# Kernel optimization log

Hardware: AMD Instinct MI355X
Metric: run time of the kernel (lower is better)

Reference implementation:

```python
import jax, jax.numpy as jnp
import numpy as np

B, H, W, IN, HID, L, M1, M2, OUT, NT = 32, 128, 256, 4, 64, 4, 12, 12, 2, 14


def setup_inputs() -> dict:
    key = jax.random.key(0)
    ks = jax.random.split(key, 32)
    f32 = jnp.float32
    n = lambda k, s, scale=0.02: jax.random.normal(k, s, dtype=f32) * scale
    inp = jax.random.normal(ks[0], (B, H, W, IN), dtype=f32)
    # ext: [B,1,6]; col0 float feature, col2 day idx in [0,8), col3 hour idx in [5,19)
    c0 = jax.random.uniform(ks[1], (B, 1), dtype=f32)
    c1 = jax.random.uniform(ks[2], (B, 1), dtype=f32)
    c2 = jax.random.randint(ks[3], (B, 1), 0, 8).astype(f32)
    c3 = jax.random.randint(ks[4], (B, 1), 5, 19).astype(f32)
    c45 = jax.random.uniform(ks[5], (B, 2), dtype=f32)
    ext = jnp.concatenate([c0, c1, c2, c3, c45], axis=1)[:, None, :]
    return {
        'inp': inp, 'ext': ext,
        'enc_w': n(ks[6], (HID, IN + 1)), 'enc_b': n(ks[7], (HID,)),
        'w1r': n(ks[8], (L, HID, HID, M1, M2), 1.0 / (HID * HID)),
        'w1i': n(ks[9], (L, HID, HID, M1, M2), 1.0 / (HID * HID)),
        'w2r': n(ks[10], (L, HID, HID, M1, M2), 1.0 / (HID * HID)),
        'w2i': n(ks[11], (L, HID, HID, M1, M2), 1.0 / (HID * HID)),
        'ws_w': n(ks[12], (L, HID, HID)), 'ws_b': n(ks[13], (L, HID)),
        'day_emb': n(ks[14], (8, 2), 1.0), 'hour_emb': n(ks[15], (24, 3), 1.0),
        'e1_w': n(ks[16], (64, 6)), 'e1_b': n(ks[17], (64,)),
        'e2_w': n(ks[18], (H * W, 64)), 'e2_b': n(ks[19], (H * W,)),
        'tw': n(ks[20], (NT, HID, HID, 3, 3)), 'tb': n(ks[21], (NT, HID)),
        'f1_w': n(ks[22], (128, HID)), 'f1_b': n(ks[23], (128,)),
        'f2_w': n(ks[24], (HID, 128)), 'f2_b': n(ks[25], (HID,)),
        'f3_w': n(ks[26], (OUT, HID)), 'f3_b': n(ks[27], (OUT,)),
    }


def _act(x):
    return jax.nn.gelu(x, approximate=False)  # torch nn.GELU default (erf)


def _spectral(x, w1, w2):
    # x: [b,c,h,w]; w1,w2: complex [c_in,c_out,M1,M2]
    b, c, h, w = x.shape
    xft = jnp.fft.rfft2(x)  # [b,c,h,w//2+1]
    out = jnp.zeros((b, w1.shape[1], h, w // 2 + 1), dtype=xft.dtype)
    out = out.at[:, :, :M1, :M2].set(
        jnp.einsum('bixy,ioxy->boxy', xft[:, :, :M1, :M2], w1))
    out = out.at[:, :, -M1:, :M2].set(
        jnp.einsum('bixy,ioxy->boxy', xft[:, :, -M1:, :M2], w2))
    return jnp.fft.irfft2(out, s=(h, w))


def reference(inp, ext, enc_w, enc_b, w1r, w1i, w2r, w2i, ws_w, ws_b,
              day_emb, hour_emb, e1_w, e1_b, e2_w, e2_b, tw, tb,
              f1_w, f1_b, f2_w, f2_b, f3_w, f3_b):
    b, h, w, _ = inp.shape
    e = ext[:, 0, :]  # squeeze(1) -> [b,6]
    # embed_ext: [ext0, day_emb, hour_emb] -> [b,6]
    emb = jnp.concatenate([
        e[:, 0:1],
        day_emb[e[:, 2].astype(jnp.int32)],
        hour_emb[e[:, 3].astype(jnp.int32)],
    ], axis=1)
    # ext2lr_global (dropout = identity in eval)
    g = _act(emb @ e1_w.T + e1_b)
    g = _act(g @ e2_w.T + e2_b).reshape(b, h, w, 1)
    x = jnp.concatenate([inp, g], axis=-1)          # [b,h,w,IN+1]
    x = (x @ enc_w.T + enc_b).transpose(0, 3, 1, 2)  # [b,HID,h,w]
    # FNO integral layers
    for i in range(L):
        x1 = _spectral(x, w1r[i] + 1j * w1i[i], w2r[i] + 1j * w2i[i])
        x2 = jnp.einsum('bchw,oc->bohw', x, ws_w[i]) + ws_b[i][None, :, None, None]
        x = x1 + x2
        if i != L - 1:
            x = _act(x)
    # decoder_time: per-sample expert conv selected by hour index
    t = e[:, 3].astype(jnp.int32) - 5  # in [0, NT)
    Wt, bt = tw[t], tb[t]              # [b,HID,HID,3,3], [b,HID]
    def one(xi, wi, bi):
        y = jax.lax.conv_general_dilated(
            xi[None], wi, (1, 1), 'SAME',
            dimension_numbers=('NCHW', 'OIHW', 'NCHW'))[0]
        return y + bi[:, None, None]
    hfeat = _act(jax.vmap(one)(x, Wt, bt)).transpose(0, 2, 3, 1)  # [b,h,w,HID]
    # decoder MLP
    z = _act(hfeat @ f1_w.T + f1_b)
    z = _act(z @ f2_w.T + f2_b)
    return z @ f3_w.T + f3_b  # [b,h,w,OUT]
```

## Files before the change

kernel.cpp:

```cpp
#include <hip/hip_runtime.h>
#include <math.h>

#define BB 32
#define HH_ 128
#define WW_ 256

typedef _Float16 f16_t;
typedef _Float16 half8 __attribute__((ext_vector_type(8)));
typedef _Float16 half4 __attribute__((ext_vector_type(4)));
typedef float floatx4 __attribute__((ext_vector_type(4)));

__device__ __forceinline__ float gelu_f(float v){
  float t = v * 0.70710678118654752f;
  float s = __builtin_fabsf(t);
  float k = __builtin_amdgcn_rcpf(__builtin_fmaf(0.3275911f, s, 1.0f));
  float p = __builtin_fmaf(1.061405429f, k, -1.453152027f);
  p = __builtin_fmaf(p, k, 1.421413741f);
  p = __builtin_fmaf(p, k, -0.284496736f);
  p = __builtin_fmaf(p, k, 0.254829592f);
  p = p * k;
  float e = __expf(-t * t);
  float erfa = __builtin_fmaf(-p, e, 1.0f);
  float er = __builtin_copysignf(erfa, v);
  float vh = 0.5f * v;
  return __builtin_fmaf(vh, er, vh);
}

__global__ void k_diag(float* out, float v){ out[threadIdx.x] = v; }

__global__ __launch_bounds__(256) void k_prep(
      float2* twf, float2* thf, float2* thi, f16_t* twzh,
      const float* __restrict__ f1_w, const float* __restrict__ f2_w,
      const float* __restrict__ f3_w, f16_t* f1T, f16_t* f2T, f16_t* f3T,
      const float* __restrict__ tw, f16_t* __restrict__ wT,
      const float* __restrict__ w1r, const float* __restrict__ w1i,
      const float* __restrict__ w2r, const float* __restrict__ w2i,
      float2* __restrict__ wmix, f16_t* __restrict__ twA){
  __shared__ __align__(16) char smp[53248];
  const double PI2 = 6.283185307179586476925286766559;
  int blk = blockIdx.x, tid = threadIdx.x;
  if (blk < 113){
    int t = blk*256 + tid;
    if (t < 3072){
      int w = t/12, ky = t%12;
      double a = -PI2 * (double)(w*ky) / 256.0;
      twf[t] = make_float2((float)cos(a), (float)sin(a));
    } else if (t < 6144){
      int f = t-3072; int h = f/24, j = f%24;
      int kx = (j<12)? j : j+104;
      double a = -PI2 * (double)(h*kx) / 128.0;
      thf[f] = make_float2((float)cos(a), (float)sin(a));
    } else if (t < 9216){
      int f = t-6144; int h = f/24, j = f%24;
      int kx = (j<12)? j : j+104;
      double a = PI2 * (double)(h*kx) / 128.0;
      thi[f] = make_float2((float)(cos(a)/128.0), (float)(sin(a)/128.0));
    } else if (t < 12288){
      int f = t-9216; int w = f/12, ky = f%12;
      double a = PI2 * (double)(w*ky) / 256.0;
      double s = (ky==0)? 1.0 : 2.0;
      twzh[w*32 + ky]      = (f16_t)( s*cos(a)/256.0);
      twzh[w*32 + 12 + ky] = (f16_t)(-s*sin(a)/256.0);
      if (ky < 8) twzh[w*32 + 24 + ky] = (f16_t)0.f;
    } else {
      int t2 = t - 12288;
      if (t2 < 8192) f1T[t2] = (f16_t)f1_w[t2];
      else if (t2 < 16384) f2T[t2-8192] = (f16_t)f2_w[t2-8192];
      else if (t2 < 16512) f3T[t2-16384] = (f16_t)f3_w[t2-16384];
    }
  } else if (blk < 169){
    float* s = (float*)smp;
    int b2 = blk - 113;
    int og = b2 & 3, tt = b2 >> 2;
    const float* src = tw + (long)tt*36864 + og*9216;
    for (int f = tid; f < 9216; f += 256) s[f] = src[f];
    __syncthreads();
    for (int f = tid; f < 9216; f += 256){
      int c = f & 63; int r = f >> 6;
      int o16 = r % 16, tap = r / 16;
      float v = s[(o16*64 + c)*9 + tap];
      wT[(((long)tt*9 + tap)*64 + og*16 + o16)*64 + c] = (f16_t)v;
    }
  } else if (blk < 937){
    float* sr = (float*)smp;
    float* si = (float*)(smp + 26624);
    int b2 = blk - 169;
    int ig  = b2 & 7;
    int kx  = (b2 >> 3) % 12;
    int sel = (b2 / 96) & 1;
    int l   = b2 / 192;
    const float* wr = sel ? w2r : w1r;
    const float* wi = sel ? w2i : w1i;
    for (int f = tid; f < 6144; f += 256){
      int i8 = f / 768; int rem = f % 768;
      int o = rem / 12, ky = rem % 12;
      long addr = (((long)l*64 + ig*8 + i8)*64 + o)*144 + kx*12 + ky;
      sr[(i8*64 + o)*13 + ky] = wr[addr];
      si[(i8*64 + o)*13 + ky] = wi[addr];
    }
    __syncthreads();
    int j = sel ? (kx + 12) : kx;
    for (int f = tid; f < 6144; f += 256){
      int o = f & 63; int r = f >> 6;
      int ky = r % 12, i8 = r / 12;
      int sidx = (i8*64 + o)*13 + ky;
      wmix[(((long)l*288 + j*12 + ky))*4096 + (ig*8 + i8)*64 + o] =
          make_float2(sr[sidx], si[sidx]);
    }
  } else {
    int t = (blk - 937)*256 + tid;
    int halfi = t >> 13, r = t & 8191;
    int hl = r >> 12, r2 = r & 4095;
    int m = r2 >> 7, k = r2 & 127;
    f16_t v = (f16_t)0.f;
    if (m < 24){
      int ky = m >> 1, ri = m & 1;
      int w = halfi*128 + k;
      double a = -PI2 * (double)(w*ky) / 256.0;
      float t32 = (float)(ri ? sin(a) : cos(a));
      f16_t hi = (f16_t)t32;
      v = hl ? (f16_t)(t32 - (float)hi) : hi;
    }
    twA[t] = v;
  }
}

__global__ __launch_bounds__(256) void k_gxdft(const float* __restrict__ ext,
      const float* __restrict__ day_emb, const float* __restrict__ hour_emb,
      const float* __restrict__ e1_w, const float* __restrict__ e1_b,
      const float* __restrict__ e2_w, const float* __restrict__ e2_b,
      const float* __restrict__ inp, const float* __restrict__ enc_w,
      const float* __restrict__ enc_b, const f16_t* __restrict__ twA,
      f16_t* __restrict__ x, float2* __restrict__ fp0, float2* __restrict__ fp1){
  __shared__ __align__(16) char sm[59392];
  f16_t* Obt   = (f16_t*)sm;
  f16_t* twA_l = (f16_t*)(sm + 35072);
  float* gvs   = (float*)(sm + 52480);
  float4* ips  = (float4*)(sm + 53504);
  float* s     = (float*)(sm + 57600);
  float* ew    = (float*)(sm + 57856);
  float* eb    = (float*)(sm + 59136);
  int tid = threadIdx.x;
  int bh = blockIdx.x;
  int b = bh >> 7, h = bh & 127;
  if (tid < 64){
    int j = tid;
    const float* e = ext + b*6;
    float emb[6];
    emb[0] = e[0];
    int d  = (int)e[2];
    emb[1] = day_emb[d*2];  emb[2] = day_emb[d*2+1];
    int hr = (int)e[3];
    emb[3] = hour_emb[hr*3]; emb[4] = hour_emb[hr*3+1]; emb[5] = hour_emb[hr*3+2];
    float acc = e1_b[j];
    #pragma unroll
    for (int k = 0; k < 6; k++) acc += emb[k]*e1_w[j*6+k];
    s[j] = gelu_f(acc);
    eb[j] = enc_b[j];
  }
  for (int f = tid; f < 320; f += 256) ew[f] = enc_w[f];
  __syncthreads();
  {
    int px = tid;
    long hw = (long)h*256 + px;
    const float4* wrow = (const float4*)(e2_w + hw*64);
    float acc = e2_b[hw];
    #pragma unroll
    for (int k = 0; k < 16; k++){
      float4 v = wrow[k];
      acc += v.x*s[4*k] + v.y*s[4*k+1] + v.z*s[4*k+2] + v.w*s[4*k+3];
    }
    gvs[px] = gelu_f(acc);
    ips[px] = *(const float4*)(inp + ((long)b*32768 + hw)*4);
  }
  __syncthreads();
  int lane = tid & 63, wv = tid >> 6;
  {
    int c = lane, wg = wv;
    const float* wr2 = ew + c*5;
    float w0 = wr2[0], w1 = wr2[1], w2 = wr2[2], w3 = wr2[3], w4 = wr2[4];
    float ebc = eb[c];
    f16_t* xo = x + ((long)bh*256 + wg*64)*64 + c;
    #pragma unroll 2
    for (int g8 = 0; g8 < 8; g8++){
      half8 hv;
      #pragma unroll
      for (int e2 = 0; e2 < 8; e2++){
        int i = g8*8 + e2;
        float4 ip = ips[wg*64 + i];
        float gv = gvs[wg*64 + i];
        float v = ebc + ip.x*w0 + ip.y*w1 + ip.z*w2 + ip.w*w3 + gv*w4;
        f16_t hval = (f16_t)v;
        hv[e2] = hval;
        xo[i*64] = hval;
      }
      *(half8*)(Obt + c*274 + wg*64 + g8*8) = hv;
    }
  }
  for (int f = tid; f < 1024; f += 256){
    int hl = f >> 9, m = (f >> 4) & 31, kc8 = f & 15;
    *(float4*)(twA_l + hl*4352 + m*136 + kc8*8) = *(const float4*)(twA + f*8);
  }
  __syncthreads();
  int n15 = lane & 15, quad = lane >> 4;
  int n = wv*16 + n15;
  #pragma unroll
  for (int half = 0; half < 2; half++){
    if (half == 1){
      __syncthreads();
      for (int f = tid; f < 1024; f += 256){
        int hl = f >> 9, m = (f >> 4) & 31, kc8 = f & 15;
        *(float4*)(twA_l + hl*4352 + m*136 + kc8*8) =
            *(const float4*)(twA + 8192 + f*8);
      }
      __syncthreads();
    }
    half8 bfr2[4];
    #pragma unroll
    for (int ks = 0; ks < 4; ks++)
      bfr2[ks] = *(const half8*)(Obt + n*274 + half*128 + ks*32 + quad*8);
    floatx4 dacc[2];
    dacc[0] = (floatx4){0.f,0.f,0.f,0.f};
    dacc[1] = (floatx4){0.f,0.f,0.f,0.f};
    #pragma unroll
    for (int hl = 0; hl < 2; hl++){
      #pragma unroll
      for (int mt = 0; mt < 2; mt++){
        #pragma unroll
        for (int ks = 0; ks < 4; ks++){
          half8 a = *(const half8*)(twA_l + hl*4352 + (mt*16 + n15)*136
                                    + ks*32 + quad*8);
          dacc[mt] = __builtin_amdgcn_mfma_f32_16x16x32_f16(a, bfr2[ks],
                                                            dacc[mt], 0,0,0);
        }
      }
    }
    float2* dst = half ? fp1 : fp0;
    #pragma unroll
    for (int mt = 0; mt < 2; mt++){
      int m0 = mt*16 + quad*4;
      if (m0 < 24){
        int ky0 = m0 >> 1;
        dst[(long)bh*768 + ky0*64 + n]     = make_float2(dacc[mt][0], dacc[mt][1]);
        dst[(long)bh*768 + (ky0+1)*64 + n] = make_float2(dacc[mt][2], dacc[mt][3]);
      }
    }
  }
}

__global__ __launch_bounds__(256) void k_spec(const float2* __restrict__ s0,
      const float2* __restrict__ s1, int dual, const float2* __restrict__ thf_g,
      const float2* __restrict__ thi_g, const float2* __restrict__ wmix,
      int layer, float2* __restrict__ zi){
  __shared__ __align__(16) char sm[40960];
  float2* th  = (float2*)sm;
  float2* xch = (float2*)(sm + 24576);
  float2* mixL= (float2*)(sm + 24576);
  int tid = threadIdx.x;
  int b = blockIdx.x / 12, ky = blockIdx.x % 12;
  int wv = tid >> 6, lane = tid & 63;
  for (int f = tid; f < 3072; f += 256) th[f] = thf_g[f];
  float2 acc[6];
  #pragma unroll
  for (int q = 0; q < 6; q++) acc[q] = make_float2(0.f, 0.f);
  long base = (long)b*98304 + ky*64;
  for (int ch = 0; ch < 4; ch++){
    __syncthreads();
    for (int f = tid; f < 2048; f += 256){
      int hh = f >> 6, c = f & 63;
      long idx = base + (long)(ch*32 + hh)*768 + c;
      float2 v = s0[idx];
      if (dual){ float2 u = s1[idx]; v.x += u.x; v.y += u.y; }
      xch[f] = v;
    }
    __syncthreads();
    for (int hh = 0; hh < 32; hh++){
      float2 v = xch[hh*64 + lane];
      int hg = ch*32 + hh;
      #pragma unroll
      for (int q = 0; q < 6; q++){
        float2 t = th[hg*24 + q*4 + wv];
        acc[q].x += t.x*v.x - t.y*v.y;
        acc[q].y += t.x*v.y + t.y*v.x;
      }
    }
  }
  __syncthreads();
  for (int f = tid; f < 3072; f += 256) th[f] = thi_g[f];
  float2 mout[6];
  #pragma unroll
  for (int q = 0; q < 6; q++){
    int j = q*4 + wv;
    const float2* wj = wmix + (((long)layer*288 + j*12 + ky))*4096;
    float re = 0.f, im = 0.f;
    #pragma unroll 8
    for (int i = 0; i < 64; i++){
      float vr = __shfl(acc[q].x, i);
      float vi = __shfl(acc[q].y, i);
      float2 ww = wj[i*64 + lane];
      re += vr*ww.x - vi*ww.y;
      im += vr*ww.y + vi*ww.x;
    }
    mout[q] = make_float2(re, im);
  }
  #pragma unroll
  for (int q = 0; q < 6; q++) mixL[(q*4 + wv)*64 + lane] = mout[q];
  __syncthreads();
  float2 cr[24];
  #pragma unroll
  for (int j = 0; j < 24; j++) cr[j] = mixL[j*64 + lane];
  for (int qq = 0; qq < 32; qq++){
    int h = qq*4 + wv;
    float re = 0.f, im = 0.f;
    #pragma unroll
    for (int j = 0; j < 24; j++){
      float2 t = th[h*24 + j];
      re += t.x*cr[j].x - t.y*cr[j].y;
      im += t.x*cr[j].y + t.y*cr[j].x;
    }
    zi[((long)b*128 + h)*768 + ky*64 + lane] = make_float2(re, im);
  }
}

__global__ __launch_bounds__(256) void k_iw_mfma(f16_t* __restrict__ x,
      const float2* __restrict__ zi, const float* __restrict__ ws_w,
      const float* __restrict__ ws_b, const f16_t* __restrict__ twzh,
      const f16_t* __restrict__ twA, float2* __restrict__ fp0,
      float2* __restrict__ fp1, int layer, int act, int dodft){
  __shared__ __align__(16) char sm[52736];
  f16_t* A  = (f16_t*)sm;
  f16_t* Bm = (f16_t*)(sm + 34816);
  float* sb = (float*)(sm + 52224);
  f16_t* Obt  = (f16_t*)sm;
  f16_t* twA_l= (f16_t*)(sm + 17408);
  int tid = threadIdx.x;
  int blk = blockIdx.x;
  int half = blk & 1;
  long bh = blk >> 1;
  int w0 = half*128;
  const f16_t* xrow = x + (bh*256 + w0)*64;
  for (int f = tid; f < 1024; f += 256){
    int px = f >> 3, c8 = (f & 7)*8;
    *(float4*)((char*)A + (px*136 + c8)*2) = *(const float4*)(xrow + px*64 + c8);
  }
  for (int f = tid; f < 4096; f += 256){
    int px = f >> 5, k = f & 31;
    if (k < 24){
      f16_t v = twzh[(w0+px)*32 + k];
      A[px*136 + 64 + k] = v;
      A[px*136 + 88 + k] = v;
      A[px*136 + 112 + k] = (f16_t)0.f;
    }
  }
  const float* wsl = ws_w + (long)layer*4096;
  for (int f = tid; f < 1024; f += 256){
    int o = f >> 4, c4 = f & 15;
    float4 v = *(const float4*)(wsl + o*64 + c4*4);
    f16_t* d = Bm + o*136 + c4*4;
    d[0]=(f16_t)v.x; d[1]=(f16_t)v.y; d[2]=(f16_t)v.z; d[3]=(f16_t)v.w;
  }
  const float2* zrow = zi + bh*768;
  for (int f = tid; f < 768; f += 256){
    int o = f & 63, ky = f >> 6;
    float2 v = zrow[ky*64 + o];
    f16_t hr = (f16_t)v.x; f16_t hi_ = (f16_t)v.y;
    Bm[o*136 + 64 + ky] = hr;
    Bm[o*136 + 76 + ky] = hi_;
    Bm[o*136 + 88 + ky] = (f16_t)(v.x - (float)hr);
    Bm[o*136 +100 + ky] = (f16_t)(v.y - (float)hi_);
  }
  for (int f = tid; f < 2048; f += 256){
    int o = f >> 5, k = f & 31;
    if (k < 24) Bm[o*136 + 112 + k] = (f16_t)0.f;
  }
  if (tid < 64) sb[tid] = ws_b[layer*64 + tid];
  __syncthreads();
  int lane = tid & 63, wv = tid >> 6;
  int n15 = lane & 15, quad = lane >> 4;
  int n = wv*16 + n15;
  half8 bfr[4];
  #pragma unroll
  for (int kc = 0; kc < 4; kc++)
    bfr[kc] = *(const half8*)(Bm + n*136 + kc*32 + quad*8);
  floatx4 acc[8];
  #pragma unroll
  for (int mt = 0; mt < 8; mt++){
    floatx4 c = {0.f,0.f,0.f,0.f};
    #pragma unroll
    for (int kc = 0; kc < 4; kc++){
      half8 a = *(const half8*)(A + (mt*16 + n15)*136 + kc*32 + quad*8);
      c = __builtin_amdgcn_mfma_f32_16x16x32_f16(a, bfr[kc], c, 0, 0, 0);
    }
    acc[mt] = c;
  }
  float bias = sb[n];
  __syncthreads();
  f16_t* xo = x + (bh*256 + w0)*64;
  #pragma unroll
  for (int mt = 0; mt < 8; mt++){
    half4 hv;
    #pragma unroll
    for (int r = 0; r < 4; r++){
      float v = acc[mt][r] + bias;
      if (act) v = gelu_f(v);
      hv[r] = (f16_t)v;
      xo[(mt*16 + quad*4 + r)*64 + n] = hv[r];
    }
    if (dodft) *(half4*)(Obt + n*136 + mt*16 + quad*4) = hv;
  }
  if (dodft){
    const f16_t* tsrc = twA + half*8192;
    for (int f = tid; f < 1024; f += 256){
      int hl = f >> 9, m = (f >> 4) & 31, kc8 = f & 15;
      *(float4*)(twA_l + hl*4352 + m*136 + kc8*8) = *(const float4*)(tsrc + f*8);
    }
    __syncthreads();
    half8 bfr2[4];
    #pragma unroll
    for (int ks = 0; ks < 4; ks++)
      bfr2[ks] = *(const half8*)(Obt + n*136 + ks*32 + quad*8);
    floatx4 dacc[2];
    dacc[0] = (floatx4){0.f,0.f,0.f,0.f};
    dacc[1] = (floatx4){0.f,0.f,0.f,0.f};
    #pragma unroll
    for (int hl = 0; hl < 2; hl++){
      #pragma unroll
      for (int mt = 0; mt < 2; mt++){
        #pragma unroll
        for (int ks = 0; ks < 4; ks++){
          half8 a = *(const half8*)(twA_l + hl*4352 + (mt*16 + n15)*136
                                    + ks*32 + quad*8);
          dacc[mt] = __builtin_amdgcn_mfma_f32_16x16x32_f16(a, bfr2[ks],
                                                            dacc[mt], 0,0,0);
        }
      }
    }
    float2* dst = half ? fp1 : fp0;
    #pragma unroll
    for (int mt = 0; mt < 2; mt++){
      int m0 = mt*16 + quad*4;
      if (m0 < 24){
        int ky0 = m0 >> 1;
        dst[bh*768 + ky0*64 + n]     = make_float2(dacc[mt][0], dacc[mt][1]);
        dst[bh*768 + (ky0+1)*64 + n] = make_float2(dacc[mt][2], dacc[mt][3]);
      }
    }
  }
}

__global__ __launch_bounds__(256) void k_conv_head(const f16_t* __restrict__ x,
      const float* __restrict__ ext, const f16_t* __restrict__ wT,
      const float* __restrict__ tb, const f16_t* __restrict__ f1T,
      const float* __restrict__ f1_b, const f16_t* __restrict__ f2T,
      const float* __restrict__ f2_b, const f16_t* __restrict__ f3T,
      const float* __restrict__ f3_b, float* __restrict__ out){
  __shared__ __align__(16) char sm[29824];
  f16_t* hf   = (f16_t*)sm;
  f16_t* z1   = (f16_t*)(sm + 9216);
  f16_t* z2   = (f16_t*)sm;
  float* tbs  = (float*)(sm + 28512);
  float* f1bs = (float*)(sm + 28768);
  float* f2bs = (float*)(sm + 29280);
  f16_t* f3s  = (f16_t*)(sm + 29536);
  float* f3bs = (float*)(sm + 29792);
  f16_t* xt   = (f16_t*)sm;

  int tid = threadIdx.x;
  int blk = blockIdx.x;
  int wc = blk & 3, h = (blk >> 2) & 127, b = blk >> 9;
  int w0 = wc*64;
  int t_idx = (int)ext[b*6+3] - 5;

  if (tid < 64) tbs[tid] = tb[t_idx*64 + tid];
  else if (tid < 192) f1bs[tid-64] = f1_b[tid-64];
  else f2bs[tid-192] = f2_b[tid-192];
  if (tid < 128) f3s[tid] = f3T[tid];
  if (tid < 2) f3bs[tid] = f3_b[tid];

  for (int f = tid; f < 1584; f += 256){
    int c8 = f & 7, r = f >> 3;
    int dy = r/66, pxl = r%66;
    int hh = h - 1 + dy, wg = w0 - 1 + pxl;
    float4 v = {0.f,0.f,0.f,0.f};
    if (hh >= 0 && hh < HH_ && wg >= 0 && wg < WW_)
      v = *(const float4*)(x + (((long)b*HH_ + hh)*WW_ + wg)*64 + c8*8);
    *(float4*)(xt + (dy*66 + pxl)*72 + c8*8) = v;
  }
  __syncthreads();

  int lane = tid & 63, wv = tid >> 6;
  int n15 = lane & 15, quad = lane >> 4;

  floatx4 acc[4];
  #pragma unroll
  for (int mt = 0; mt < 4; mt++) acc[mt] = (floatx4){0.f,0.f,0.f,0.f};
  const f16_t* wTt = wT + (long)t_idx*36864;
  for (int tap = 0; tap < 9; tap++){
    int dy = tap/3, dx = tap%3;
    const f16_t* wrow = wTt + (tap*64 + wv*16 + n15)*64;
    #pragma unroll
    for (int kc = 0; kc < 2; kc++){
      half8 bfrag = *(const half8*)(wrow + kc*32 + quad*8);
      #pragma unroll
      for (int mt = 0; mt < 4; mt++){
        int p = mt*16 + n15 + dx;
        half8 a = *(const half8*)(xt + (dy*66 + p)*72 + kc*32 + quad*8);
        acc[mt] = __builtin_amdgcn_mfma_f32_16x16x32_f16(a, bfrag, acc[mt], 0,0,0);
      }
    }
  }
  __syncthreads();
  {
    int n = wv*16 + n15;
    float bias = tbs[n];
    #pragma unroll
    for (int mt = 0; mt < 4; mt++){
      #pragma unroll
      for (int r = 0; r < 4; r++){
        int m = mt*16 + quad*4 + r;
        hf[m*72 + n] = (f16_t)gelu_f(acc[mt][r] + bias);
      }
    }
  }
  __syncthreads();
  #pragma unroll
  for (int nt = 0; nt < 2; nt++){
    int n = wv*32 + nt*16 + n15;
    float bias = f1bs[n];
    half8 bf0 = *(const half8*)(f1T + n*64 + quad*8);
    half8 bf1 = *(const half8*)(f1T + n*64 + 32 + quad*8);
    #pragma unroll
    for (int mt = 0; mt < 4; mt++){
      floatx4 c = {0.f,0.f,0.f,0.f};
      half8 a0 = *(const half8*)(hf + (mt*16 + n15)*72 + quad*8);
      half8 a1 = *(const half8*)(hf + (mt*16 + n15)*72 + 32 + quad*8);
      c = __builtin_amdgcn_mfma_f32_16x16x32_f16(a0, bf0, c, 0,0,0);
      c = __builtin_amdgcn_mfma_f32_16x16x32_f16(a1, bf1, c, 0,0,0);
      #pragma unroll
      for (int r = 0; r < 4; r++){
        int m = mt*16 + quad*4 + r;
        z1[m*136 + n] = (f16_t)gelu_f(c[r] + bias);
      }
    }
  }
  __syncthreads();
  {
    int n = wv*16 + n15;
    float bias = f2bs[n];
    half8 bf[4];
    #pragma unroll
    for (int kc = 0; kc < 4; kc++)
      bf[kc] = *(const half8*)(f2T + n*128 + kc*32 + quad*8);
    #pragma unroll
    for (int mt = 0; mt < 4; mt++){
      floatx4 c = {0.f,0.f,0.f,0.f};
      #pragma unroll
      for (int kc = 0; kc < 4; kc++){
        half8 a = *(const half8*)(z1 + (mt*16 + n15)*136 + kc*32 + quad*8);
        c = __builtin_amdgcn_mfma_f32_16x16x32_f16(a, bf[kc], c, 0,0,0);
      }
      #pragma unroll
      for (int r = 0; r < 4; r++){
        int m = mt*16 + quad*4 + r;
        z2[m*72 + n] = (f16_t)gelu_f(c[r] + bias);
      }
    }
  }
  __syncthreads();
  if (tid < 128){
    int px = tid >> 1, oo = tid & 1;
    const f16_t* zr = z2 + px*72;
    const f16_t* fr = f3s + oo*64;
    float a = f3bs[oo];
    #pragma unroll
    for (int g = 0; g < 8; g++){
      half8 zv = *(const half8*)(zr + g*8);
      half8 wv2 = *(const half8*)(fr + g*8);
      #pragma unroll
      for (int q = 0; q < 8; q++) a += (float)zv[q]*(float)wv2[q];
    }
    out[(((long)b*HH_ + h)*WW_ + w0 + px)*2 + oo] = a;
  }
}

extern "C" void kernel_launch(void* const* d_in, const int* in_sizes, int n_in,
                              void* d_out, int out_size, void* d_ws, size_t ws_size,
                              hipStream_t stream){
  const float* inp     = (const float*)d_in[0];
  const float* ext     = (const float*)d_in[1];
  const float* enc_w   = (const float*)d_in[2];
  const float* enc_b   = (const float*)d_in[3];
  const float* w1r     = (const float*)d_in[4];
  const float* w1i     = (const float*)d_in[5];
  const float* w2r     = (const float*)d_in[6];
  const float* w2i     = (const float*)d_in[7];
  const float* ws_w    = (const float*)d_in[8];
  const float* ws_b    = (const float*)d_in[9];
  const float* day_emb = (const float*)d_in[10];
  const float* hour_emb= (const float*)d_in[11];
  const float* e1_w    = (const float*)d_in[12];
  const float* e1_b    = (const float*)d_in[13];
  const float* e2_w    = (const float*)d_in[14];
  const float* e2_b    = (const float*)d_in[15];
  const float* tw      = (const float*)d_in[16];
  const float* tb      = (const float*)d_in[17];
  const float* f1_w    = (const float*)d_in[18];
  const float* f1_b    = (const float*)d_in[19];
  const float* f2_w    = (const float*)d_in[20];
  const float* f2_b    = (const float*)d_in[21];
  const float* f3_w    = (const float*)d_in[22];
  const float* f3_b    = (const float*)d_in[23];
  float* outp = (float*)d_out;

  const size_t need = 248652032;
  if (ws_size < need){
    k_diag<<<dim3(1), dim3(64), 0, stream>>>(outp, (float)(ws_size >> 20));
    return;
  }
  char* p = (char*)d_ws;
  f16_t*  x    = (f16_t*)(p);
  float2* fp0  = (float2*)(p + 134217728);
  float2* fp1  = (float2*)(p + 159383552);
  float2* zi   = (float2*)(p + 184549376);
  float2* twf  = (float2*)(p + 209715200);
  float2* thf  = (float2*)(p + 209739776);
  float2* thi  = (float2*)(p + 209764352);
  f16_t*  twzh = (f16_t*)(p + 209788928);
  f16_t*  wT   = (f16_t*)(p + 209805312);
  f16_t*  f1T  = (f16_t*)(p + 210837504);
  f16_t*  f2T  = (f16_t*)(p + 210853888);
  f16_t*  f3T  = (f16_t*)(p + 210870272);
  float2* wmix = (float2*)(p + 210870528);
  f16_t*  twA  = (f16_t*)(p + 248619264);

  k_prep<<<dim3(1001), dim3(256), 0, stream>>>(twf, thf, thi, twzh,
      f1_w, f2_w, f3_w, f1T, f2T, f3T, tw, wT, w1r, w1i, w2r, w2i, wmix, twA);
  k_gxdft<<<dim3(4096), dim3(256), 0, stream>>>(ext, day_emb, hour_emb,
      e1_w, e1_b, e2_w, e2_b, inp, enc_w, enc_b, twA, x, fp0, fp1);
  for (int l = 0; l < 4; l++){
    k_spec<<<dim3(384), dim3(256), 0, stream>>>(fp0, fp1, 1,
                                                thf, thi, wmix, l, zi);
    k_iw_mfma<<<dim3(8192), dim3(256), 0, stream>>>(x, zi, ws_w, ws_b, twzh,
                       twA, fp0, fp1, l, (l < 3) ? 1 : 0, (l < 3) ? 1 : 0);
  }
  k_conv_head<<<dim3(16384), dim3(256), 0, stream>>>(x, ext, wT, tb,
                     f1T, f1_b, f2T, f2_b, f3T, f3_b, outp);
}
```

Measured before the change: 1.289 ms.

## Read DFT twiddles from global, restructure integral-layer MFMA, trim LDS and GELU

After: 1.200 ms. 6.9% less time.

```diff
diff --git a/kernel.cpp b/kernel.cpp
--- a/kernel.cpp
+++ b/kernel.cpp
@@ -8,22 +8,21 @@
 typedef _Float16 f16_t;
 typedef _Float16 half8 __attribute__((ext_vector_type(8)));
 typedef _Float16 half4 __attribute__((ext_vector_type(4)));
+typedef _Float16 half2v __attribute__((ext_vector_type(2)));
 typedef float floatx4 __attribute__((ext_vector_type(4)));
 
 __device__ __forceinline__ float gelu_f(float v){
-  float t = v * 0.70710678118654752f;
-  float s = __builtin_fabsf(t);
+  float av = __builtin_fabsf(v);
+  float s = av * 0.70710678118654752f;
   float k = __builtin_amdgcn_rcpf(__builtin_fmaf(0.3275911f, s, 1.0f));
   float p = __builtin_fmaf(1.061405429f, k, -1.453152027f);
   p = __builtin_fmaf(p, k, 1.421413741f);
   p = __builtin_fmaf(p, k, -0.284496736f);
   p = __builtin_fmaf(p, k, 0.254829592f);
   p = p * k;
-  float e = __expf(-t * t);
-  float erfa = __builtin_fmaf(-p, e, 1.0f);
-  float er = __builtin_copysignf(erfa, v);
-  float vh = 0.5f * v;
-  return __builtin_fmaf(vh, er, vh);
+  float e = __expf(-s * s);
+  float q = 0.5f * av * p;
+  return __builtin_fmaf(-q, e, fmaxf(v, 0.f));
 }
 
 __global__ void k_diag(float* out, float v){ out[threadIdx.x] = v; }
@@ -132,14 +131,13 @@
       const float* __restrict__ inp, const float* __restrict__ enc_w,
       const float* __restrict__ enc_b, const f16_t* __restrict__ twA,
       f16_t* __restrict__ x, float2* __restrict__ fp0, float2* __restrict__ fp1){
-  __shared__ __align__(16) char sm[59392];
+  __shared__ __align__(16) char sm[41984];
   f16_t* Obt   = (f16_t*)sm;
-  f16_t* twA_l = (f16_t*)(sm + 35072);
-  float* gvs   = (float*)(sm + 52480);
-  float4* ips  = (float4*)(sm + 53504);
-  float* s     = (float*)(sm + 57600);
-  float* ew    = (float*)(sm + 57856);
-  float* eb    = (float*)(sm + 59136);
+  float* gvs   = (float*)(sm + 35072);
+  float4* ips  = (float4*)(sm + 36096);
+  float* s     = (float*)(sm + 40192);
+  float* ew    = (float*)(sm + 40448);
+  float* eb    = (float*)(sm + 41728);
   int tid = threadIdx.x;
   int bh = blockIdx.x;
   int b = bh >> 7, h = bh & 127;
@@ -197,24 +195,11 @@
       *(half8*)(Obt + c*274 + wg*64 + g8*8) = hv;
     }
   }
-  for (int f = tid; f < 1024; f += 256){
-    int hl = f >> 9, m = (f >> 4) & 31, kc8 = f & 15;
-    *(float4*)(twA_l + hl*4352 + m*136 + kc8*8) = *(const float4*)(twA + f*8);
-  }
   __syncthreads();
   int n15 = lane & 15, quad = lane >> 4;
   int n = wv*16 + n15;
   #pragma unroll
   for (int half = 0; half < 2; half++){
-    if (half == 1){
-      __syncthreads();
-      for (int f = tid; f < 1024; f += 256){
-        int hl = f >> 9, m = (f >> 4) & 31, kc8 = f & 15;
-        *(float4*)(twA_l + hl*4352 + m*136 + kc8*8) =
-            *(const float4*)(twA + 8192 + f*8);
-      }
-      __syncthreads();
-    }
     half8 bfr2[4];
     #pragma unroll
     for (int ks = 0; ks < 4; ks++)
@@ -228,8 +213,8 @@
       for (int mt = 0; mt < 2; mt++){
         #pragma unroll
         for (int ks = 0; ks < 4; ks++){
-          half8 a = *(const half8*)(twA_l + hl*4352 + (mt*16 + n15)*136
-                                    + ks*32 + quad*8);
+          half8 a = *(const half8*)(twA + half*8192 + hl*4096
+                                    + (mt*16 + n15)*128 + ks*32 + quad*8);
           dacc[mt] = __builtin_amdgcn_mfma_f32_16x16x32_f16(a, bfr2[ks],
                                                             dacc[mt], 0,0,0);
         }
@@ -327,12 +312,11 @@
       const float* __restrict__ ws_b, const f16_t* __restrict__ twzh,
       const f16_t* __restrict__ twA, float2* __restrict__ fp0,
       float2* __restrict__ fp1, int layer, int act, int dodft){
-  __shared__ __align__(16) char sm[52736];
-  f16_t* A  = (f16_t*)sm;
-  f16_t* Bm = (f16_t*)(sm + 34816);
-  float* sb = (float*)(sm + 52224);
-  f16_t* Obt  = (f16_t*)sm;
-  f16_t* twA_l= (f16_t*)(sm + 17408);
+  __shared__ __align__(16) char sm[28672];
+  f16_t* A1  = (f16_t*)sm;
+  f16_t* Bzh = (f16_t*)(sm + 18432);
+  f16_t* Bzl = (f16_t*)(sm + 23552);
+  f16_t* Obt = (f16_t*)sm;
   int tid = threadIdx.x;
   int blk = blockIdx.x;
   int half = blk & 1;
@@ -340,60 +324,57 @@
   int w0 = half*128;
   const f16_t* xrow = x + (bh*256 + w0)*64;
   for (int f = tid; f < 1024; f += 256){
-    int px = f >> 3, c8 = (f & 7)*8;
-    *(float4*)((char*)A + (px*136 + c8)*2) = *(const float4*)(xrow + px*64 + c8);
-  }
-  for (int f = tid; f < 4096; f += 256){
-    int px = f >> 5, k = f & 31;
-    if (k < 24){
-      f16_t v = twzh[(w0+px)*32 + k];
-      A[px*136 + 64 + k] = v;
-      A[px*136 + 88 + k] = v;
-      A[px*136 + 112 + k] = (f16_t)0.f;
-    }
-  }
-  const float* wsl = ws_w + (long)layer*4096;
-  for (int f = tid; f < 1024; f += 256){
-    int o = f >> 4, c4 = f & 15;
-    float4 v = *(const float4*)(wsl + o*64 + c4*4);
-    f16_t* d = Bm + o*136 + c4*4;
-    d[0]=(f16_t)v.x; d[1]=(f16_t)v.y; d[2]=(f16_t)v.z; d[3]=(f16_t)v.w;
+    int px = f >> 3, c8 = f & 7;
+    *(float4*)(A1 + px*72 + c8*8) = *(const float4*)(xrow + px*64 + c8*8);
   }
   const float2* zrow = zi + bh*768;
   for (int f = tid; f < 768; f += 256){
     int o = f & 63, ky = f >> 6;
     float2 v = zrow[ky*64 + o];
     f16_t hr = (f16_t)v.x; f16_t hi_ = (f16_t)v.y;
-    Bm[o*136 + 64 + ky] = hr;
-    Bm[o*136 + 76 + ky] = hi_;
-    Bm[o*136 + 88 + ky] = (f16_t)(v.x - (float)hr);
-    Bm[o*136 +100 + ky] = (f16_t)(v.y - (float)hi_);
-  }
-  for (int f = tid; f < 2048; f += 256){
-    int o = f >> 5, k = f & 31;
-    if (k < 24) Bm[o*136 + 112 + k] = (f16_t)0.f;
-  }
-  if (tid < 64) sb[tid] = ws_b[layer*64 + tid];
+    Bzh[o*40 + ky]      = hr;
+    Bzh[o*40 + 12 + ky] = hi_;
+    Bzl[o*40 + ky]      = (f16_t)(v.x - (float)hr);
+    Bzl[o*40 + 12 + ky] = (f16_t)(v.y - (float)hi_);
+  }
+  if (tid < 64){
+    float4 z4 = {0.f,0.f,0.f,0.f};
+    *(float4*)(Bzh + tid*40 + 24) = z4;
+    *(float4*)(Bzl + tid*40 + 24) = z4;
+  }
   __syncthreads();
   int lane = tid & 63, wv = tid >> 6;
   int n15 = lane & 15, quad = lane >> 4;
   int n = wv*16 + n15;
-  half8 bfr[4];
-  #pragma unroll
-  for (int kc = 0; kc < 4; kc++)
-    bfr[kc] = *(const half8*)(Bm + n*136 + kc*32 + quad*8);
+  half8 bws[2];
+  {
+    const float* wsl = ws_w + ((long)layer*64 + n)*64;
+    #pragma unroll
+    for (int kc = 0; kc < 2; kc++){
+      float4 u0 = *(const float4*)(wsl + kc*32 + quad*8);
+      float4 u1 = *(const float4*)(wsl + kc*32 + quad*8 + 4);
+      half8 hb;
+      hb[0]=(f16_t)u0.x; hb[1]=(f16_t)u0.y; hb[2]=(f16_t)u0.z; hb[3]=(f16_t)u0.w;
+      hb[4]=(f16_t)u1.x; hb[5]=(f16_t)u1.y; hb[6]=(f16_t)u1.z; hb[7]=(f16_t)u1.w;
+      bws[kc] = hb;
+    }
+  }
+  half8 bzh = *(const half8*)(Bzh + n*40 + quad*8);
+  half8 bzl = *(const half8*)(Bzl + n*40 + quad*8);
   floatx4 acc[8];
   #pragma unroll
   for (int mt = 0; mt < 8; mt++){
     floatx4 c = {0.f,0.f,0.f,0.f};
-    #pragma unroll
-    for (int kc = 0; kc < 4; kc++){
-      half8 a = *(const half8*)(A + (mt*16 + n15)*136 + kc*32 + quad*8);
-      c = __builtin_amdgcn_mfma_f32_16x16x32_f16(a, bfr[kc], c, 0, 0, 0);
-    }
+    half8 ax0 = *(const half8*)(A1 + (mt*16 + n15)*72 + quad*8);
+    half8 ax1 = *(const half8*)(A1 + (mt*16 + n15)*72 + 32 + quad*8);
+    half8 atw = *(const half8*)(twzh + (w0 + mt*16 + n15)*32 + quad*8);
+    c = __builtin_amdgcn_mfma_f32_16x16x32_f16(ax0, bws[0], c, 0,0,0);
+    c = __builtin_amdgcn_mfma_f32_16x16x32_f16(ax1, bws[1], c, 0,0,0);
+    c = __builtin_amdgcn_mfma_f32_16x16x32_f16(atw, bzh,    c, 0,0,0);
+    c = __builtin_amdgcn_mfma_f32_16x16x32_f16(atw, bzl,    c, 0,0,0);
     acc[mt] = c;
   }
-  float bias = sb[n];
+  float bias = ws_b[layer*64 + n];
   __syncthreads();
   f16_t* xo = x + (bh*256 + w0)*64;
   #pragma unroll
@@ -409,11 +390,6 @@
     if (dodft) *(half4*)(Obt + n*136 + mt*16 + quad*4) = hv;
   }
   if (dodft){
-    const f16_t* tsrc = twA + half*8192;
-    for (int f = tid; f < 1024; f += 256){
-      int hl = f >> 9, m = (f >> 4) & 31, kc8 = f & 15;
-      *(float4*)(twA_l + hl*4352 + m*136 + kc8*8) = *(const float4*)(tsrc + f*8);
-    }
     __syncthreads();
     half8 bfr2[4];
     #pragma unroll
@@ -428,8 +404,8 @@
       for (int mt = 0; mt < 2; mt++){
         #pragma unroll
         for (int ks = 0; ks < 4; ks++){
-          half8 a = *(const half8*)(twA_l + hl*4352 + (mt*16 + n15)*136
-                                    + ks*32 + quad*8);
+          half8 a = *(const half8*)(twA + half*8192 + hl*4096
+                                    + (mt*16 + n15)*128 + ks*32 + quad*8);
           dacc[mt] = __builtin_amdgcn_mfma_f32_16x16x32_f16(a, bfr2[ks],
                                                             dacc[mt], 0,0,0);
         }
@@ -477,9 +453,18 @@
   if (tid < 128) f3s[tid] = f3T[tid];
   if (tid < 2) f3bs[tid] = f3_b[tid];
 
-  for (int f = tid; f < 1584; f += 256){
-    int c8 = f & 7, r = f >> 3;
-    int dy = r/66, pxl = r%66;
+  for (int f = tid; f < 1536; f += 256){
+    int c8 = f & 7, px = (f >> 3) & 63, dy = f >> 9;
+    int hh = h - 1 + dy;
+    float4 v = {0.f,0.f,0.f,0.f};
+    if (hh >= 0 && hh < HH_)
+      v = *(const float4*)(x + (((long)b*HH_ + hh)*WW_ + w0 + px)*64 + c8*8);
+    *(float4*)(xt + (dy*66 + px + 1)*72 + c8*8) = v;
+  }
+  if (tid < 48){
+    int c8 = tid & 7, r = tid >> 3;
+    int dy = r >> 1, side = r & 1;
+    int pxl = side ? 65 : 0;
     int hh = h - 1 + dy, wg = w0 - 1 + pxl;
     float4 v = {0.f,0.f,0.f,0.f};
     if (hh >= 0 && hh < HH_ && wg >= 0 && wg < WW_)
@@ -576,8 +561,17 @@
     for (int g = 0; g < 8; g++){
       half8 zv = *(const half8*)(zr + g*8);
       half8 wv2 = *(const half8*)(fr + g*8);
+#if __has_builtin(__builtin_amdgcn_fdot2)
+      #pragma unroll
+      for (int q = 0; q < 4; q++){
+        half2v za = {zv[2*q], zv[2*q+1]};
+        half2v wa = {wv2[2*q], wv2[2*q+1]};
+        a = __builtin_amdgcn_fdot2(za, wa, a, false);
+      }
+#else
       #pragma unroll
       for (int q = 0; q < 8; q++) a += (float)zv[q]*(float)wv2[q];
+#endif
     }
     out[(((long)b*HH_ + h)*WW_ + w0 + px)*2 + oo] = a;
   }
```
